# Performance work log

Hardware: AMD Instinct MI355X
Metric: run time of the kernel (lower is better)

The kernel has to match this reference:

```python
import jax, jax.numpy as jnp
import numpy as np

DIM = 256
HEADS = 8
HD = DIM // HEADS  # 32
RPE_H = 512
STRIDE = 16
B, NQ = 4, 300
HH, WW = 64, 64
N = HH * WW


def setup_inputs() -> dict:
    key = jax.random.key(0)
    ks = jax.random.split(key, 24)

    def lin(k, fan_in, fan_out):
        return (jax.random.normal(k, (fan_in, fan_out), jnp.float32)
                / np.float32(np.sqrt(fan_in)))

    # boxes in absolute pixel coords (image is WW*STRIDE = 1024 px wide)
    rp_xy = jax.random.uniform(ks[0], (B, NQ, 1, 2), jnp.float32) * (WW * STRIDE)
    rp_wh = jax.random.uniform(ks[1], (B, NQ, 1, 2), jnp.float32) * 256.0 + 16.0
    reference_points = jnp.concatenate([rp_xy, rp_wh], axis=-1)  # [B,NQ,1,4]

    inp = {
        "query": jax.random.normal(ks[2], (B, NQ, DIM), jnp.float32),
        "reference_points": reference_points,
        "k_input_flatten": jax.random.normal(ks[3], (B, N, DIM), jnp.float32),
        "v_input_flatten": jax.random.normal(ks[4], (B, N, DIM), jnp.float32),
        "input_spatial_shapes": jnp.array([[HH, WW]], dtype=jnp.int32),
        "input_padding_mask": (jax.random.uniform(ks[5], (B, N)) < 0.1).astype(jnp.int32),
        # projections (stored as [in, out]; y = x @ W + b)
        "Wq": lin(ks[6], DIM, DIM), "bq": jnp.zeros((DIM,), jnp.float32),
        "Wk": lin(ks[7], DIM, DIM), "bk": jnp.zeros((DIM,), jnp.float32),
        "Wv": lin(ks[8], DIM, DIM), "bv": jnp.zeros((DIM,), jnp.float32),
        "Wp": lin(ks[9], DIM, DIM), "bp": jnp.zeros((DIM,), jnp.float32),
        # CPB MLP 1 (x-deltas): Linear(2,512)+ReLU+Linear(512,HEADS,no bias)
        "W1x": lin(ks[10], 2, RPE_H), "b1x": jnp.zeros((RPE_H,), jnp.float32),
        "W2x": lin(ks[11], RPE_H, HEADS),
        # CPB MLP 2 (y-deltas)
        "W1y": lin(ks[12], 2, RPE_H), "b1y": jnp.zeros((RPE_H,), jnp.float32),
        "W2y": lin(ks[13], RPE_H, HEADS),
    }
    return inp


def reference(query, reference_points, k_input_flatten, v_input_flatten,
              input_spatial_shapes, input_padding_mask,
              Wq, bq, Wk, bk, Wv, bv, Wp, bp,
              W1x, b1x, W2x, W1y, b1y, W2y):
    h = int(input_spatial_shapes[0, 0])
    w = int(input_spatial_shapes[0, 1])
    scale = HD ** -0.5

    # cxcywh -> (x1,y1,x2,y2)
    c, s = reference_points[..., :2], reference_points[..., 2:]
    ref_pts = jnp.concatenate([c - s / 2, c + s / 2], axis=-1)  # [B,NQ,1,4]

    pos_x = (jnp.arange(w, dtype=jnp.float32) + 0.5) * STRIDE  # [w]
    pos_y = (jnp.arange(h, dtype=jnp.float32) + 0.5) * STRIDE  # [h]
    delta_x = ref_pts[..., 0::2] - pos_x[None, None, :, None]  # [B,NQ,w,2]
    delta_y = ref_pts[..., 1::2] - pos_y[None, None, :, None]  # [B,NQ,h,2]

    rpe_x = jax.nn.relu(delta_x @ W1x + b1x) @ W2x  # [B,NQ,w,HEADS]
    rpe_y = jax.nn.relu(delta_y @ W1y + b1y) @ W2y  # [B,NQ,h,HEADS]
    rpe = rpe_x[:, :, None, :, :] + rpe_y[:, :, :, None, :]  # [B,NQ,h,w,H]

    Bq, Nq, C = query.shape
    rpe = rpe.reshape(Bq, Nq, h * w, HEADS).transpose(0, 3, 1, 2)  # [B,H,NQ,N]

    q = (query @ Wq + bq).reshape(Bq, Nq, HEADS, HD).transpose(0, 2, 1, 3) * scale
    k = (k_input_flatten @ Wk + bk).reshape(Bq, -1, HEADS, HD).transpose(0, 2, 1, 3)
    v = (v_input_flatten @ Wv + bv).reshape(Bq, -1, HEADS, HD).transpose(0, 2, 1, 3)

    attn = jnp.einsum('bhqd,bhkd->bhqk', q, k) + rpe
    attn = attn + input_padding_mask[:, None, None, :].astype(attn.dtype) * (-100.0)
    fi = jnp.finfo(attn.dtype)
    attn = jnp.clip(attn, fi.min, fi.max)
    attn = jax.nn.softmax(attn, axis=-1)

    x = jnp.einsum('bhqk,bhkd->bhqd', attn, v)
    x = x.transpose(0, 2, 1, 3).reshape(Bq, Nq, C)
    return x @ Wp + bp
```

## Files before the change

kernel.cpp:

```cpp
#include <hip/hip_runtime.h>
#include <math.h>

#define B_   4
#define NQ_  300
#define DIM_ 256
#define H_   8
#define HD_  32
#define N_   4096

typedef _Float16 f16;
typedef f16   f16x8 __attribute__((ext_vector_type(8)));
typedef f16   f16x4 __attribute__((ext_vector_type(4)));
typedef float f32x4 __attribute__((ext_vector_type(4)));

#define L2E 1.44269504f

__global__ __launch_bounds__(256) void prep_wt(
    const float* __restrict__ Wq, const float* __restrict__ Wk,
    const float* __restrict__ Wv, const float* __restrict__ Wp,
    const int* __restrict__ mask, f16* __restrict__ WT,
    float* __restrict__ maskf, float qscale)
{
  const int z = blockIdx.z;
  if (z == 4) {
    const int flat = blockIdx.y * 4 + blockIdx.x;
    const int idx = flat * 1024 + threadIdx.x * 4;
    int4 mm = *(const int4*)(mask + idx);
    float4 o;
    o.x = -100.f * L2E * (float)mm.x;
    o.y = -100.f * L2E * (float)mm.y;
    o.z = -100.f * L2E * (float)mm.z;
    o.w = -100.f * L2E * (float)mm.w;
    *(float4*)(maskf + idx) = o;
    return;
  }
  __shared__ float t[64][65];
  const float* W = z == 0 ? Wq : z == 1 ? Wk : z == 2 ? Wv : Wp;
  const float s = z == 0 ? qscale : 1.0f;
  f16* O = WT + (size_t)z * 65536;
  const int k0 = blockIdx.y * 64, n0 = blockIdx.x * 64;
  const int r = threadIdx.x >> 2, c0 = (threadIdx.x & 3) * 16;
#pragma unroll
  for (int c = 0; c < 16; c += 4) {
    float4 v = *(const float4*)(W + (size_t)(k0 + r) * 256 + n0 + c0 + c);
    t[r][c0 + c] = v.x; t[r][c0 + c + 1] = v.y;
    t[r][c0 + c + 2] = v.z; t[r][c0 + c + 3] = v.w;
  }
  __syncthreads();
  f16* orow = O + (size_t)(n0 + r) * 256 + k0 + c0;
#pragma unroll
  for (int c = 0; c < 16; c += 4) {
    f16x4 p;
    p[0] = (f16)(t[c0 + c + 0][r] * s);
    p[1] = (f16)(t[c0 + c + 1][r] * s);
    p[2] = (f16)(t[c0 + c + 2][r] * s);
    p[3] = (f16)(t[c0 + c + 3][r] * s);
    *(f16x4*)(orow + c) = p;
  }
}

__device__ __forceinline__ void gemm_body(
    const void* __restrict__ Ain, const f16* __restrict__ WT,
    const float* __restrict__ bias, void* __restrict__ C,
    int M, int a_f16, int mode, int bm, int bn, int tid)
{
  __shared__ f16 As[128][40];
  __shared__ f16 Bs[64][40];
  __shared__ f16 Ts[64][132];
  const int lane = tid & 63;
  const int wv = tid >> 6;
  const int l15 = lane & 15, g = lane >> 4;

  f32x4 acc[2][4];
#pragma unroll
  for (int mt = 0; mt < 2; ++mt)
#pragma unroll
    for (int nt = 0; nt < 4; ++nt) acc[mt][nt] = (f32x4){0.f, 0.f, 0.f, 0.f};

  for (int k0 = 0; k0 < 256; k0 += 32) {
#pragma unroll
    for (int i = 0; i < 2; ++i) {
      const int c = tid + i * 256;
      const int row = c >> 2, k8 = (c & 3) * 8;
      const int gm = bm + row;
      f16x8 av;
      if (gm < M) {
        if (a_f16) {
          av = *(const f16x8*)((const f16*)Ain + (size_t)gm * 256 + k0 + k8);
        } else {
          const float* ap = (const float*)Ain + (size_t)gm * 256 + k0 + k8;
          float4 a0 = *(const float4*)ap;
          float4 a1 = *(const float4*)(ap + 4);
          av[0] = (f16)a0.x; av[1] = (f16)a0.y; av[2] = (f16)a0.z; av[3] = (f16)a0.w;
          av[4] = (f16)a1.x; av[5] = (f16)a1.y; av[6] = (f16)a1.z; av[7] = (f16)a1.w;
        }
      } else {
#pragma unroll
        for (int j = 0; j < 8; ++j) av[j] = (f16)0.f;
      }
      *(f16x8*)&As[row][k8] = av;
    }
    {
      const int n = tid >> 2, k8 = (tid & 3) * 8;
      *(f16x8*)&Bs[n][k8] = *(const f16x8*)(WT + (size_t)(bn + n) * 256 + k0 + k8);
    }
    __syncthreads();
    const f16x8 af0 = *(const f16x8*)&As[wv * 32 + l15][g * 8];
    const f16x8 af1 = *(const f16x8*)&As[wv * 32 + 16 + l15][g * 8];
#pragma unroll
    for (int nt = 0; nt < 4; ++nt) {
      const f16x8 bf = *(const f16x8*)&Bs[nt * 16 + l15][g * 8];
      acc[0][nt] = __builtin_amdgcn_mfma_f32_16x16x32_f16(af0, bf, acc[0][nt], 0, 0, 0);
      acc[1][nt] = __builtin_amdgcn_mfma_f32_16x16x32_f16(af1, bf, acc[1][nt], 0, 0, 0);
    }
    __syncthreads();
  }

  if (mode == 2) {
#pragma unroll
    for (int nt = 0; nt < 4; ++nt) {
      const float bv = bias[bn + nt * 16 + l15];
#pragma unroll
      for (int mt = 0; mt < 2; ++mt)
#pragma unroll
        for (int r = 0; r < 4; ++r)
          Ts[nt * 16 + l15][wv * 32 + mt * 16 + g * 4 + r] = (f16)(acc[mt][nt][r] + bv);
    }
    __syncthreads();
    const int n = tid >> 2, mc = (tid & 3) * 32;
    const int bb = bm >> 12, nk0 = bm & 4095;
    f16* dst = (f16*)C + (size_t)bb * (256 * 4096) +
               (size_t)(bn + n) * 4096 + nk0 + mc;
#pragma unroll
    for (int j = 0; j < 4; ++j)
      *(f16x8*)(dst + j * 8) = *(const f16x8*)&Ts[n][mc + j * 8];
  } else {
#pragma unroll
    for (int nt = 0; nt < 4; ++nt) {
      const int n = bn + nt * 16 + l15;
      const float bv = bias[n];
#pragma unroll
      for (int mt = 0; mt < 2; ++mt)
#pragma unroll
      for (int r = 0; r < 4; ++r) {
        const int m = bm + wv * 32 + mt * 16 + g * 4 + r;
        if (m >= M) continue;
        const float v = acc[mt][nt][r] + bv;
        if (mode == 0) ((float*)C)[(size_t)m * 256 + n] = v;
        else           ((f16*)C)[(size_t)m * 256 + n] = (f16)v;
      }
    }
  }
}

__global__ __launch_bounds__(256) void proj_qkv(
    const float* __restrict__ query, const float* __restrict__ kin,
    const float* __restrict__ vin, const f16* __restrict__ WT,
    const float* __restrict__ bq, const float* __restrict__ bk,
    const float* __restrict__ bv, f16* __restrict__ Qf,
    f16* __restrict__ Kf, f16* __restrict__ Vtf)
{
  const int z = blockIdx.z;
  const int bm = blockIdx.y * 128, bn = blockIdx.x * 64;
  if (z == 0) {
    if (bm >= B_ * NQ_) return;
    gemm_body(query, WT, bq, Qf, B_ * NQ_, 0, 1, bm, bn, threadIdx.x);
  } else if (z == 1) {
    gemm_body(kin, WT + 65536, bk, Kf, B_ * N_, 0, 1, bm, bn, threadIdx.x);
  } else {
    gemm_body(vin, WT + 2 * 65536, bv, Vtf, B_ * N_, 0, 2, bm, bn, threadIdx.x);
  }
}

__global__ __launch_bounds__(256) void gemm_out(
    const f16* __restrict__ X, const f16* __restrict__ WT,
    const float* __restrict__ bp, float* __restrict__ out)
{
  gemm_body(X, WT + 3 * 65536, bp, out, B_ * NQ_, 1, 0,
            blockIdx.y * 128, blockIdx.x * 64, threadIdx.x);
}

__global__ __launch_bounds__(256) void rpe_kernel(
    const float* __restrict__ refpts,
    const float* __restrict__ W1x, const float* __restrict__ b1x, const float* __restrict__ W2x,
    const float* __restrict__ W1y, const float* __restrict__ b1y, const float* __restrict__ W2y,
    float* __restrict__ rpxT, float* __restrict__ rpyT)
{
  __shared__ float sRed[4][64][9];
  const int tid = threadIdx.x;
  const int lane = tid & 63;
  const int wv = __builtin_amdgcn_readfirstlane(tid >> 6);
  const int bq = blockIdx.x;
  const int axis = blockIdx.y;
  const float* W1 = axis ? W1y : W1x;
  const float* b1 = axis ? b1y : b1x;
  const float* W2 = axis ? W2y : W2x;
  float* out = axis ? rpyT : rpxT;
  const int b = bq / NQ_, q = bq % NQ_;

  const float c  = refpts[bq * 4 + axis];
  const float sz = refpts[bq * 4 + 2 + axis];
  const float pos = (lane + 0.5f) * 16.0f;
  const float d0 = c - 0.5f * sz - pos;
  const float d1 = c + 0.5f * sz - pos;
  float acc[8] = {};
  const int r0 = wv * 128;
#pragma unroll 4
  for (int i = 0; i < 128; ++i) {
    const int r = r0 + i;
    const float w10 = W1[r], w11 = W1[512 + r], bb = b1[r];
    const float hv = fmaxf(fmaf(d0, w10, fmaf(d1, w11, bb)), 0.0f);
    const float* w2r = W2 + r * 8;
#pragma unroll
    for (int hh = 0; hh < 8; ++hh) acc[hh] += hv * w2r[hh];
  }
#pragma unroll
  for (int hh = 0; hh < 8; ++hh) sRed[wv][lane][hh] = acc[hh];
  __syncthreads();
  for (int idx = tid; idx < 512; idx += 256) {
    const int hh = idx >> 6, jj = idx & 63;
    out[((size_t)(b * H_ + hh) * NQ_ + q) * 64 + jj] =
        (sRed[0][jj][hh] + sRed[1][jj][hh] + sRed[2][jj][hh] + sRed[3][jj][hh]) * L2E;
  }
}

__global__ __launch_bounds__(512, 4) void attn_mfma(
    const f16* __restrict__ Qf, const f16* __restrict__ Kf,
    const f16* __restrict__ Vtf, const float* __restrict__ rpxT,
    const float* __restrict__ rpyT, const float* __restrict__ maskf,
    f16* __restrict__ X)
{
  __shared__ float srx[32][68];
  __shared__ float sry[32][68];
  __shared__ float pm[8][2][64];
  __shared__ f16x4 mO4[7][4][64];
  __shared__ float mll[7][32];

  const int tid = threadIdx.x;
  const int lane = tid & 63;
  const int kh = tid >> 6;
  const int qg = blockIdx.x % 10;
  const int h  = (blockIdx.x / 10) % H_;
  const int b  = blockIdx.x / (10 * H_);
  const int q0 = qg * 32;

  {
    const int qq = tid >> 4, j4 = tid & 15;
    int qa = q0 + qq; if (qa > NQ_ - 1) qa = NQ_ - 1;
    const size_t base = ((size_t)((b * H_ + h) * NQ_ + qa)) * 64 + j4 * 4;
    *(float4*)&srx[qq][j4 * 4] = *(const float4*)(rpxT + base);
    *(float4*)&sry[qq][j4 * 4] = *(const float4*)(rpyT + base);
  }
  __syncthreads();

  const int l15 = lane & 15, g = lane >> 4;
  const int qrow0 = q0 + l15;
  const int qrow1 = q0 + 16 + l15;
  const int qa = qrow0 > NQ_ - 1 ? NQ_ - 1 : qrow0;
  const int qb = qrow1 > NQ_ - 1 ? NQ_ - 1 : qrow1;

  const f16x8 qf0 = *(const f16x8*)(Qf + (size_t)(b * NQ_ + qa) * 256 + h * 32 + g * 8);
  const f16x8 qf1 = *(const f16x8*)(Qf + (size_t)(b * NQ_ + qb) * 256 + h * 32 + g * 8);

  const f16* kb  = Kf + (size_t)b * N_ * 256 + h * 32 + g * 8;
  const f16* v0p = Vtf + (size_t)(b * 256 + h * 32 + l15) * N_ + g * 4;
  const f16* v1p = v0p + (size_t)16 * N_;
  const float* mb = maskf + b * N_;

  float cmax0 = -1e30f, cmax1 = -1e30f;
  for (int sp = 0; sp < 8; ++sp) {
    const int kbase = kh * 512 + sp * 64;
    f16x8 kf[4]; float4 m4[4];
#pragma unroll
    for (int cc = 0; cc < 4; ++cc) {
      kf[cc] = *(const f16x8*)(kb + (size_t)(kbase + cc * 16 + l15) * 256);
      m4[cc] = *(const float4*)(mb + kbase + cc * 16 + g * 4);
    }
    const float ry0 = sry[l15][kbase >> 6];
    const float ry1 = sry[16 + l15][kbase >> 6];
#pragma unroll
    for (int cc = 0; cc < 4; ++cc) {
      f32x4 S0 = __builtin_amdgcn_mfma_f32_16x16x32_f16(
          kf[cc], qf0, (f32x4){0.f, 0.f, 0.f, 0.f}, 0, 0, 0);
      f32x4 S1 = __builtin_amdgcn_mfma_f32_16x16x32_f16(
          kf[cc], qf1, (f32x4){0.f, 0.f, 0.f, 0.f}, 0, 0, 0);
      const float4 rx0 = *(const float4*)&srx[l15][cc * 16 + g * 4];
      const float4 rx1 = *(const float4*)&srx[16 + l15][cc * 16 + g * 4];
      cmax0 = fmaxf(cmax0, fmaxf(
          fmaxf(fmaf(S0[0], L2E, rx0.x + m4[cc].x + ry0),
                fmaf(S0[1], L2E, rx0.y + m4[cc].y + ry0)),
          fmaxf(fmaf(S0[2], L2E, rx0.z + m4[cc].z + ry0),
                fmaf(S0[3], L2E, rx0.w + m4[cc].w + ry0))));
      cmax1 = fmaxf(cmax1, fmaxf(
          fmaxf(fmaf(S1[0], L2E, rx1.x + m4[cc].x + ry1),
                fmaf(S1[1], L2E, rx1.y + m4[cc].y + ry1)),
          fmaxf(fmaf(S1[2], L2E, rx1.z + m4[cc].z + ry1),
                fmaf(S1[3], L2E, rx1.w + m4[cc].w + ry1))));
    }
  }
  pm[kh][0][lane] = cmax0;
  pm[kh][1][lane] = cmax1;
  __syncthreads();
  float m0 = -1e30f, m1 = -1e30f;
#pragma unroll
  for (int w = 0; w < 8; ++w)
#pragma unroll
    for (int gg = 0; gg < 4; ++gg) {
      m0 = fmaxf(m0, pm[w][0][gg * 16 + l15]);
      m1 = fmaxf(m1, pm[w][1][gg * 16 + l15]);
    }

  f32x4 O00 = {0.f,0.f,0.f,0.f}, O01 = {0.f,0.f,0.f,0.f};
  f32x4 O10 = {0.f,0.f,0.f,0.f}, O11 = {0.f,0.f,0.f,0.f};
  float lacc0 = 0.f, lacc1 = 0.f;
  for (int sp = 0; sp < 8; ++sp) {
    const int kbase = kh * 512 + sp * 64;
    f16x8 kf[4]; f16x4 va[4], vb[4]; float4 m4[4];
#pragma unroll
    for (int cc = 0; cc < 4; ++cc) {
      kf[cc] = *(const f16x8*)(kb + (size_t)(kbase + cc * 16 + l15) * 256);
      va[cc] = *(const f16x4*)(v0p + kbase + cc * 16);
      vb[cc] = *(const f16x4*)(v1p + kbase + cc * 16);
      m4[cc] = *(const float4*)(mb + kbase + cc * 16 + g * 4);
    }
    const float ry0 = sry[l15][kbase >> 6] - m0;
    const float ry1 = sry[16 + l15][kbase >> 6] - m1;
#pragma unroll
    for (int cc = 0; cc < 4; ++cc) {
      f32x4 S0 = __builtin_amdgcn_mfma_f32_16x16x32_f16(
          kf[cc], qf0, (f32x4){0.f, 0.f, 0.f, 0.f}, 0, 0, 0);
      f32x4 S1 = __builtin_amdgcn_mfma_f32_16x16x32_f16(
          kf[cc], qf1, (f32x4){0.f, 0.f, 0.f, 0.f}, 0, 0, 0);
      const float4 rx0 = *(const float4*)&srx[l15][cc * 16 + g * 4];
      const float4 rx1 = *(const float4*)&srx[16 + l15][cc * 16 + g * 4];
      f16x4 pf0, pf1;
      {
        const float p0 = exp2f(fmaf(S0[0], L2E, rx0.x + m4[cc].x + ry0));
        const float p1 = exp2f(fmaf(S0[1], L2E, rx0.y + m4[cc].y + ry0));
        const float p2 = exp2f(fmaf(S0[2], L2E, rx0.z + m4[cc].z + ry0));
        const float p3 = exp2f(fmaf(S0[3], L2E, rx0.w + m4[cc].w + ry0));
        lacc0 += p0 + p1 + p2 + p3;
        pf0[0] = (f16)p0; pf0[1] = (f16)p1; pf0[2] = (f16)p2; pf0[3] = (f16)p3;
      }
      {
        const float p0 = exp2f(fmaf(S1[0], L2E, rx1.x + m4[cc].x + ry1));
        const float p1 = exp2f(fmaf(S1[1], L2E, rx1.y + m4[cc].y + ry1));
        const float p2 = exp2f(fmaf(S1[2], L2E, rx1.z + m4[cc].z + ry1));
        const float p3 = exp2f(fmaf(S1[3], L2E, rx1.w + m4[cc].w + ry1));
        lacc1 += p0 + p1 + p2 + p3;
        pf1[0] = (f16)p0; pf1[1] = (f16)p1; pf1[2] = (f16)p2; pf1[3] = (f16)p3;
      }
      O00 = __builtin_amdgcn_mfma_f32_16x16x16f16(va[cc], pf0, O00, 0, 0, 0);
      O01 = __builtin_amdgcn_mfma_f32_16x16x16f16(vb[cc], pf0, O01, 0, 0, 0);
      O10 = __builtin_amdgcn_mfma_f32_16x16x16f16(va[cc], pf1, O10, 0, 0, 0);
      O11 = __builtin_amdgcn_mfma_f32_16x16x16f16(vb[cc], pf1, O11, 0, 0, 0);
    }
  }
  lacc0 += __shfl_xor(lacc0, 16); lacc0 += __shfl_xor(lacc0, 32);
  lacc1 += __shfl_xor(lacc1, 16); lacc1 += __shfl_xor(lacc1, 32);

  if (kh > 0) {
    f16x4 t;
#pragma unroll
    for (int r = 0; r < 4; ++r) t[r] = (f16)O00[r];
    mO4[kh - 1][0][lane] = t;
#pragma unroll
    for (int r = 0; r < 4; ++r) t[r] = (f16)O01[r];
    mO4[kh - 1][1][lane] = t;
#pragma unroll
    for (int r = 0; r < 4; ++r) t[r] = (f16)O10[r];
    mO4[kh - 1][2][lane] = t;
#pragma unroll
    for (int r = 0; r < 4; ++r) t[r] = (f16)O11[r];
    mO4[kh - 1][3][lane] = t;
    if (lane < 16) {
      mll[kh - 1][lane]      = lacc0;
      mll[kh - 1][16 + lane] = lacc1;
    }
  }
  __syncthreads();
  if (kh == 0) {
    float lt0 = lacc0, lt1 = lacc1;
#pragma unroll
    for (int w = 0; w < 7; ++w) {
      lt0 += mll[w][l15];
      lt1 += mll[w][16 + l15];
#pragma unroll
      for (int r = 0; r < 4; ++r) {
        O00[r] += (float)mO4[w][0][lane][r];
        O01[r] += (float)mO4[w][1][lane][r];
        O10[r] += (float)mO4[w][2][lane][r];
        O11[r] += (float)mO4[w][3][lane][r];
      }
    }
    const float rl0 = 1.0f / lt0;
    const float rl1 = 1.0f / lt1;
    if (qrow0 < NQ_) {
      f16* xr = X + (size_t)(b * NQ_ + qrow0) * 256 + h * 32;
      f16x4 p0, p1;
#pragma unroll
      for (int r = 0; r < 4; ++r) {
        p0[r] = (f16)(O00[r] * rl0);
        p1[r] = (f16)(O01[r] * rl0);
      }
      *(f16x4*)(xr + g * 4) = p0;
      *(f16x4*)(xr + 16 + g * 4) = p1;
    }
    if (qrow1 < NQ_) {
      f16* xr = X + (size_t)(b * NQ_ + qrow1) * 256 + h * 32;
      f16x4 p0, p1;
#pragma unroll
      for (int r = 0; r < 4; ++r) {
        p0[r] = (f16)(O10[r] * rl1);
        p1[r] = (f16)(O11[r] * rl1);
      }
      *(f16x4*)(xr + g * 4) = p0;
      *(f16x4*)(xr + 16 + g * 4) = p1;
    }
  }
}

extern "C" void kernel_launch(void* const* d_in, const int* in_sizes, int n_in,
                              void* d_out, int out_size, void* d_ws, size_t ws_size,
                              hipStream_t stream)
{
  const float* query  = (const float*)d_in[0];
  const float* refpts = (const float*)d_in[1];
  const float* kin    = (const float*)d_in[2];
  const float* vin    = (const float*)d_in[3];
  const int*   mask   = (const int*)d_in[5];
  const float* Wq = (const float*)d_in[6];
  const float* bq = (const float*)d_in[7];
  const float* Wk = (const float*)d_in[8];
  const float* bk = (const float*)d_in[9];
  const float* Wv = (const float*)d_in[10];
  const float* bv = (const float*)d_in[11];
  const float* Wp = (const float*)d_in[12];
  const float* bp = (const float*)d_in[13];
  const float* W1x = (const float*)d_in[14];
  const float* b1x = (const float*)d_in[15];
  const float* W2x = (const float*)d_in[16];
  const float* W1y = (const float*)d_in[17];
  const float* b1y = (const float*)d_in[18];
  const float* W2y = (const float*)d_in[19];

  char* wsb = (char*)d_ws;
  f16*   Qf    = (f16*)(wsb);
  f16*   Kf    = (f16*)(wsb + 655360);
  f16*   Vtf   = (f16*)(wsb + 9043968);
  float* rpxT  = (float*)(wsb + 17432576);
  float* rpyT  = (float*)(wsb + 19890176);
  f16*   X     = (f16*)(wsb + 22347776);
  f16*   WT    = (f16*)(wsb + 23003136);
  float* maskf = (float*)(wsb + 23527424);

  const float scale = 0.17677669529663687f;

  hipLaunchKernelGGL(prep_wt, dim3(4, 4, 5), dim3(256), 0, stream,
                     Wq, Wk, Wv, Wp, mask, WT, maskf, scale);
  hipLaunchKernelGGL(rpe_kernel, dim3(B_ * NQ_, 2), dim3(256), 0, stream,
                     refpts, W1x, b1x, W2x, W1y, b1y, W2y, rpxT, rpyT);
  hipLaunchKernelGGL(proj_qkv, dim3(4, 128, 3), dim3(256), 0, stream,
                     query, kin, vin, WT, bq, bk, bv, Qf, Kf, Vtf);
  hipLaunchKernelGGL(attn_mfma, dim3(B_ * H_ * 10), dim3(512), 0, stream,
                     Qf, Kf, Vtf, rpxT, rpyT, maskf, X);
  hipLaunchKernelGGL(gemm_out, dim3(4, 10), dim3(256), 0, stream,
                     X, WT, bp, (float*)d_out);
}
```

Baseline: 251.2 us.

## Replace two-pass softmax with online softmax and split keys across two blocks

Removes the separate max-finding pass over K in the attention kernel and uses an online (running-max) softmax with rescaling, so K/QK^T are computed once instead of twice. The key range is also split between two blocks per query group, which doubles the grid to 640 blocks, and a new merge kernel combines the partial outputs using the log-sum-exp factors. Partials are written to the workspace as fp32. This adds an extra launch, per-tile rescaling work and partial-result traffic. The launch-bounds occupancy hint is dropped.

```diff
diff --git a/kernel.cpp b/kernel.cpp
--- a/kernel.cpp
+++ b/kernel.cpp
@@ -224,30 +224,33 @@
   }
 }
 
-__global__ __launch_bounds__(512, 4) void attn_mfma(
+__global__ __launch_bounds__(512) void attn_mfma(
     const f16* __restrict__ Qf, const f16* __restrict__ Kf,
     const f16* __restrict__ Vtf, const float* __restrict__ rpxT,
     const float* __restrict__ rpyT, const float* __restrict__ maskf,
-    f16* __restrict__ X)
+    float* __restrict__ pO, float* __restrict__ pml)
 {
   __shared__ float srx[32][68];
   __shared__ float sry[32][68];
-  __shared__ float pm[8][2][64];
   __shared__ f16x4 mO4[7][4][64];
+  __shared__ float mlm[7][32];
   __shared__ float mll[7][32];
 
   const int tid = threadIdx.x;
   const int lane = tid & 63;
-  const int kh = tid >> 6;
-  const int qg = blockIdx.x % 10;
-  const int h  = (blockIdx.x / 10) % H_;
-  const int b  = blockIdx.x / (10 * H_);
+  const int kw = tid >> 6;
+  const int bid = blockIdx.x;
+  const int KH = bid & 1;
+  const int rest = bid >> 1;
+  const int qg = rest % 10;
+  const int h  = (rest / 10) % H_;
+  const int b  = rest / (10 * H_);
   const int q0 = qg * 32;
 
   {
     const int qq = tid >> 4, j4 = tid & 15;
-    int qa = q0 + qq; if (qa > NQ_ - 1) qa = NQ_ - 1;
-    const size_t base = ((size_t)((b * H_ + h) * NQ_ + qa)) * 64 + j4 * 4;
+    int qa2 = q0 + qq; if (qa2 > NQ_ - 1) qa2 = NQ_ - 1;
+    const size_t base = ((size_t)((b * H_ + h) * NQ_ + qa2)) * 64 + j4 * 4;
     *(float4*)&srx[qq][j4 * 4] = *(const float4*)(rpxT + base);
     *(float4*)&sry[qq][j4 * 4] = *(const float4*)(rpyT + base);
   }
@@ -262,59 +265,17 @@
   const f16x8 qf0 = *(const f16x8*)(Qf + (size_t)(b * NQ_ + qa) * 256 + h * 32 + g * 8);
   const f16x8 qf1 = *(const f16x8*)(Qf + (size_t)(b * NQ_ + qb) * 256 + h * 32 + g * 8);
 
+  f32x4 O00 = {0.f,0.f,0.f,0.f}, O01 = {0.f,0.f,0.f,0.f};
+  f32x4 O10 = {0.f,0.f,0.f,0.f}, O11 = {0.f,0.f,0.f,0.f};
+  float lacc0 = 0.f, lacc1 = 0.f;
+  float mrun0 = -1e30f, mrun1 = -1e30f;
   const f16* kb  = Kf + (size_t)b * N_ * 256 + h * 32 + g * 8;
   const f16* v0p = Vtf + (size_t)(b * 256 + h * 32 + l15) * N_ + g * 4;
   const f16* v1p = v0p + (size_t)16 * N_;
   const float* mb = maskf + b * N_;
 
-  float cmax0 = -1e30f, cmax1 = -1e30f;
-  for (int sp = 0; sp < 8; ++sp) {
-    const int kbase = kh * 512 + sp * 64;
-    f16x8 kf[4]; float4 m4[4];
-#pragma unroll
-    for (int cc = 0; cc < 4; ++cc) {
-      kf[cc] = *(const f16x8*)(kb + (size_t)(kbase + cc * 16 + l15) * 256);
-      m4[cc] = *(const float4*)(mb + kbase + cc * 16 + g * 4);
-    }
-    const float ry0 = sry[l15][kbase >> 6];
-    const float ry1 = sry[16 + l15][kbase >> 6];
-#pragma unroll
-    for (int cc = 0; cc < 4; ++cc) {
-      f32x4 S0 = __builtin_amdgcn_mfma_f32_16x16x32_f16(
-          kf[cc], qf0, (f32x4){0.f, 0.f, 0.f, 0.f}, 0, 0, 0);
-      f32x4 S1 = __builtin_amdgcn_mfma_f32_16x16x32_f16(
-          kf[cc], qf1, (f32x4){0.f, 0.f, 0.f, 0.f}, 0, 0, 0);
-      const float4 rx0 = *(const float4*)&srx[l15][cc * 16 + g * 4];
-      const float4 rx1 = *(const float4*)&srx[16 + l15][cc * 16 + g * 4];
-      cmax0 = fmaxf(cmax0, fmaxf(
-          fmaxf(fmaf(S0[0], L2E, rx0.x + m4[cc].x + ry0),
-                fmaf(S0[1], L2E, rx0.y + m4[cc].y + ry0)),
-          fmaxf(fmaf(S0[2], L2E, rx0.z + m4[cc].z + ry0),
-                fmaf(S0[3], L2E, rx0.w + m4[cc].w + ry0))));
-      cmax1 = fmaxf(cmax1, fmaxf(
-          fmaxf(fmaf(S1[0], L2E, rx1.x + m4[cc].x + ry1),
-                fmaf(S1[1], L2E, rx1.y + m4[cc].y + ry1)),
-          fmaxf(fmaf(S1[2], L2E, rx1.z + m4[cc].z + ry1),
-                fmaf(S1[3], L2E, rx1.w + m4[cc].w + ry1))));
-    }
-  }
-  pm[kh][0][lane] = cmax0;
-  pm[kh][1][lane] = cmax1;
-  __syncthreads();
-  float m0 = -1e30f, m1 = -1e30f;
-#pragma unroll
-  for (int w = 0; w < 8; ++w)
-#pragma unroll
-    for (int gg = 0; gg < 4; ++gg) {
-      m0 = fmaxf(m0, pm[w][0][gg * 16 + l15]);
-      m1 = fmaxf(m1, pm[w][1][gg * 16 + l15]);
-    }
-
-  f32x4 O00 = {0.f,0.f,0.f,0.f}, O01 = {0.f,0.f,0.f,0.f};
-  f32x4 O10 = {0.f,0.f,0.f,0.f}, O11 = {0.f,0.f,0.f,0.f};
-  float lacc0 = 0.f, lacc1 = 0.f;
-  for (int sp = 0; sp < 8; ++sp) {
-    const int kbase = kh * 512 + sp * 64;
+  for (int sp = 0; sp < 4; ++sp) {
+    const int kbase = KH * 2048 + kw * 256 + sp * 64;
     f16x8 kf[4]; f16x4 va[4], vb[4]; float4 m4[4];
 #pragma unroll
     for (int cc = 0; cc < 4; ++cc) {
@@ -323,32 +284,53 @@
       vb[cc] = *(const f16x4*)(v1p + kbase + cc * 16);
       m4[cc] = *(const float4*)(mb + kbase + cc * 16 + g * 4);
     }
-    const float ry0 = sry[l15][kbase >> 6] - m0;
-    const float ry1 = sry[16 + l15][kbase >> 6] - m1;
+    f32x4 s0[4], s1[4];
+    float lm0 = -1e30f, lm1 = -1e30f;
+    const float ry0 = sry[l15][kbase >> 6];
+    const float ry1 = sry[16 + l15][kbase >> 6];
 #pragma unroll
     for (int cc = 0; cc < 4; ++cc) {
       f32x4 S0 = __builtin_amdgcn_mfma_f32_16x16x32_f16(
-          kf[cc], qf0, (f32x4){0.f, 0.f, 0.f, 0.f}, 0, 0, 0);
+          kf[cc], qf0, (f32x4){0.f,0.f,0.f,0.f}, 0, 0, 0);
       f32x4 S1 = __builtin_amdgcn_mfma_f32_16x16x32_f16(
-          kf[cc], qf1, (f32x4){0.f, 0.f, 0.f, 0.f}, 0, 0, 0);
+          kf[cc], qf1, (f32x4){0.f,0.f,0.f,0.f}, 0, 0, 0);
       const float4 rx0 = *(const float4*)&srx[l15][cc * 16 + g * 4];
       const float4 rx1 = *(const float4*)&srx[16 + l15][cc * 16 + g * 4];
+      s0[cc][0] = fmaf(S0[0], L2E, rx0.x + m4[cc].x + ry0);
+      s0[cc][1] = fmaf(S0[1], L2E, rx0.y + m4[cc].y + ry0);
+      s0[cc][2] = fmaf(S0[2], L2E, rx0.z + m4[cc].z + ry0);
+      s0[cc][3] = fmaf(S0[3], L2E, rx0.w + m4[cc].w + ry0);
+      s1[cc][0] = fmaf(S1[0], L2E, rx1.x + m4[cc].x + ry1);
+      s1[cc][1] = fmaf(S1[1], L2E, rx1.y + m4[cc].y + ry1);
+      s1[cc][2] = fmaf(S1[2], L2E, rx1.z + m4[cc].z + ry1);
+      s1[cc][3] = fmaf(S1[3], L2E, rx1.w + m4[cc].w + ry1);
+      lm0 = fmaxf(lm0, fmaxf(fmaxf(s0[cc][0], s0[cc][1]), fmaxf(s0[cc][2], s0[cc][3])));
+      lm1 = fmaxf(lm1, fmaxf(fmaxf(s1[cc][0], s1[cc][1]), fmaxf(s1[cc][2], s1[cc][3])));
+    }
+    lm0 = fmaxf(lm0, __shfl_xor(lm0, 16));
+    lm0 = fmaxf(lm0, __shfl_xor(lm0, 32));
+    lm1 = fmaxf(lm1, __shfl_xor(lm1, 16));
+    lm1 = fmaxf(lm1, __shfl_xor(lm1, 32));
+    const float mn0 = fmaxf(mrun0, lm0);
+    const float mn1 = fmaxf(mrun1, lm1);
+    const float f0 = exp2f(mrun0 - mn0);
+    const float f1 = exp2f(mrun1 - mn1);
+    mrun0 = mn0; mrun1 = mn1;
+    lacc0 *= f0; lacc1 *= f1;
+#pragma unroll
+    for (int r = 0; r < 4; ++r) {
+      O00[r] *= f0; O01[r] *= f0;
+      O10[r] *= f1; O11[r] *= f1;
+    }
+#pragma unroll
+    for (int cc = 0; cc < 4; ++cc) {
       f16x4 pf0, pf1;
-      {
-        const float p0 = exp2f(fmaf(S0[0], L2E, rx0.x + m4[cc].x + ry0));
-        const float p1 = exp2f(fmaf(S0[1], L2E, rx0.y + m4[cc].y + ry0));
-        const float p2 = exp2f(fmaf(S0[2], L2E, rx0.z + m4[cc].z + ry0));
-        const float p3 = exp2f(fmaf(S0[3], L2E, rx0.w + m4[cc].w + ry0));
-        lacc0 += p0 + p1 + p2 + p3;
-        pf0[0] = (f16)p0; pf0[1] = (f16)p1; pf0[2] = (f16)p2; pf0[3] = (f16)p3;
-      }
-      {
-        const float p0 = exp2f(fmaf(S1[0], L2E, rx1.x + m4[cc].x + ry1));
-        const float p1 = exp2f(fmaf(S1[1], L2E, rx1.y + m4[cc].y + ry1));
-        const float p2 = exp2f(fmaf(S1[2], L2E, rx1.z + m4[cc].z + ry1));
-        const float p3 = exp2f(fmaf(S1[3], L2E, rx1.w + m4[cc].w + ry1));
-        lacc1 += p0 + p1 + p2 + p3;
-        pf1[0] = (f16)p0; pf1[1] = (f16)p1; pf1[2] = (f16)p2; pf1[3] = (f16)p3;
+#pragma unroll
+      for (int r = 0; r < 4; ++r) {
+        const float p0 = exp2f(s0[cc][r] - mrun0);
+        const float p1 = exp2f(s1[cc][r] - mrun1);
+        lacc0 += p0; lacc1 += p1;
+        pf0[r] = (f16)p0; pf1[r] = (f16)p1;
       }
       O00 = __builtin_amdgcn_mfma_f32_16x16x16f16(va[cc], pf0, O00, 0, 0, 0);
       O01 = __builtin_amdgcn_mfma_f32_16x16x16f16(vb[cc], pf0, O01, 0, 0, 0);
@@ -356,67 +338,107 @@
       O11 = __builtin_amdgcn_mfma_f32_16x16x16f16(vb[cc], pf1, O11, 0, 0, 0);
     }
   }
+
   lacc0 += __shfl_xor(lacc0, 16); lacc0 += __shfl_xor(lacc0, 32);
   lacc1 += __shfl_xor(lacc1, 16); lacc1 += __shfl_xor(lacc1, 32);
 
-  if (kh > 0) {
+  if (kw > 0) {
     f16x4 t;
 #pragma unroll
     for (int r = 0; r < 4; ++r) t[r] = (f16)O00[r];
-    mO4[kh - 1][0][lane] = t;
+    mO4[kw - 1][0][lane] = t;
 #pragma unroll
     for (int r = 0; r < 4; ++r) t[r] = (f16)O01[r];
-    mO4[kh - 1][1][lane] = t;
+    mO4[kw - 1][1][lane] = t;
 #pragma unroll
     for (int r = 0; r < 4; ++r) t[r] = (f16)O10[r];
-    mO4[kh - 1][2][lane] = t;
+    mO4[kw - 1][2][lane] = t;
 #pragma unroll
     for (int r = 0; r < 4; ++r) t[r] = (f16)O11[r];
-    mO4[kh - 1][3][lane] = t;
+    mO4[kw - 1][3][lane] = t;
     if (lane < 16) {
-      mll[kh - 1][lane]      = lacc0;
-      mll[kh - 1][16 + lane] = lacc1;
+      mlm[kw - 1][lane]      = mrun0;
+      mlm[kw - 1][16 + lane] = mrun1;
+      mll[kw - 1][lane]      = lacc0;
+      mll[kw - 1][16 + lane] = lacc1;
     }
   }
   __syncthreads();
-  if (kh == 0) {
-    float lt0 = lacc0, lt1 = lacc1;
+  if (kw == 0) {
+    float ms0 = mrun0, ms1 = mrun1;
 #pragma unroll
     for (int w = 0; w < 7; ++w) {
-      lt0 += mll[w][l15];
-      lt1 += mll[w][16 + l15];
+      ms0 = fmaxf(ms0, mlm[w][l15]);
+      ms1 = fmaxf(ms1, mlm[w][16 + l15]);
+    }
+    const float fs0 = exp2f(mrun0 - ms0);
+    const float fs1 = exp2f(mrun1 - ms1);
+    float lt0 = lacc0 * fs0, lt1 = lacc1 * fs1;
+#pragma unroll
+    for (int r = 0; r < 4; ++r) {
+      O00[r] *= fs0; O01[r] *= fs0;
+      O10[r] *= fs1; O11[r] *= fs1;
+    }
+#pragma unroll
+    for (int w = 0; w < 7; ++w) {
+      const float fw0 = exp2f(mlm[w][l15] - ms0);
+      const float fw1 = exp2f(mlm[w][16 + l15] - ms1);
+      lt0 += mll[w][l15] * fw0;
+      lt1 += mll[w][16 + l15] * fw1;
 #pragma unroll
       for (int r = 0; r < 4; ++r) {
-        O00[r] += (float)mO4[w][0][lane][r];
-        O01[r] += (float)mO4[w][1][lane][r];
-        O10[r] += (float)mO4[w][2][lane][r];
-        O11[r] += (float)mO4[w][3][lane][r];
+        O00[r] += (float)mO4[w][0][lane][r] * fw0;
+        O01[r] += (float)mO4[w][1][lane][r] * fw0;
+        O10[r] += (float)mO4[w][2][lane][r] * fw1;
+        O11[r] += (float)mO4[w][3][lane][r] * fw1;
       }
     }
-    const float rl0 = 1.0f / lt0;
-    const float rl1 = 1.0f / lt1;
-    if (qrow0 < NQ_) {
-      f16* xr = X + (size_t)(b * NQ_ + qrow0) * 256 + h * 32;
-      f16x4 p0, p1;
-#pragma unroll
-      for (int r = 0; r < 4; ++r) {
-        p0[r] = (f16)(O00[r] * rl0);
-        p1[r] = (f16)(O01[r] * rl0);
-      }
-      *(f16x4*)(xr + g * 4) = p0;
-      *(f16x4*)(xr + 16 + g * 4) = p1;
-    }
-    if (qrow1 < NQ_) {
-      f16* xr = X + (size_t)(b * NQ_ + qrow1) * 256 + h * 32;
-      f16x4 p0, p1;
-#pragma unroll
-      for (int r = 0; r < 4; ++r) {
-        p0[r] = (f16)(O10[r] * rl1);
-        p1[r] = (f16)(O11[r] * rl1);
-      }
-      *(f16x4*)(xr + g * 4) = p0;
-      *(f16x4*)(xr + 16 + g * 4) = p1;
-    }
+    float4* pO4 = (float4*)pO;
+    const size_t pb2 = ((size_t)rest * 2 + KH) * 4 * 64;
+    pO4[pb2 + 0 * 64 + lane] = make_float4(O00[0], O00[1], O00[2], O00[3]);
+    pO4[pb2 + 1 * 64 + lane] = make_float4(O01[0], O01[1], O01[2], O01[3]);
+    pO4[pb2 + 2 * 64 + lane] = make_float4(O10[0], O10[1], O10[2], O10[3]);
+    pO4[pb2 + 3 * 64 + lane] = make_float4(O11[0], O11[1], O11[2], O11[3]);
+    if (lane < 16) {
+      float* pp = pml + ((size_t)rest * 2 + KH) * 64;
+      pp[l15]      = ms0;
+      pp[16 + l15] = lt0;
+      pp[32 + l15] = ms1;
+      pp[48 + l15] = lt1;
+    }
+  }
+}
+
+__global__ __launch_bounds__(256) void attn_merge(
+    const float* __restrict__ pO, const float* __restrict__ pml,
+    f16* __restrict__ X)
+{
+  const int pb = blockIdx.x;
+  const int qg = pb % 10;
+  const int h  = (pb / 10) % H_;
+  const int b  = pb / (10 * H_);
+  const int t = threadIdx.x;
+  const int qt = t >> 7, oh = (t >> 6) & 1, lane = t & 63;
+  const int l15 = lane & 15, g = lane >> 4;
+
+  const float4* pO4 = (const float4*)pO;
+  const float4 a = pO4[(((size_t)pb * 2 + 0) * 4 + qt * 2 + oh) * 64 + lane];
+  const float4 c = pO4[(((size_t)pb * 2 + 1) * 4 + qt * 2 + oh) * 64 + lane];
+  const float* pp0 = pml + ((size_t)pb * 2 + 0) * 64 + qt * 32;
+  const float* pp1 = pml + ((size_t)pb * 2 + 1) * 64 + qt * 32;
+  const float m0 = pp0[l15], l0 = pp0[16 + l15];
+  const float m1 = pp1[l15], l1 = pp1[16 + l15];
+  const float ms = fmaxf(m0, m1);
+  const float f0 = exp2f(m0 - ms), f1 = exp2f(m1 - ms);
+  const float rl = 1.0f / (l0 * f0 + l1 * f1);
+  const int qrow = qg * 32 + qt * 16 + l15;
+  if (qrow < NQ_) {
+    f16x4 o;
+    o[0] = (f16)((a.x * f0 + c.x * f1) * rl);
+    o[1] = (f16)((a.y * f0 + c.y * f1) * rl);
+    o[2] = (f16)((a.z * f0 + c.z * f1) * rl);
+    o[3] = (f16)((a.w * f0 + c.w * f1) * rl);
+    *(f16x4*)(X + (size_t)(b * NQ_ + qrow) * 256 + h * 32 + oh * 16 + g * 4) = o;
   }
 }
 
@@ -453,6 +475,8 @@
   f16*   X     = (f16*)(wsb + 22347776);
   f16*   WT    = (f16*)(wsb + 23003136);
   float* maskf = (float*)(wsb + 23527424);
+  float* pO    = (float*)(wsb + 23592960);
+  float* pml   = (float*)(wsb + 26214400);
 
   const float scale = 0.17677669529663687f;
 
@@ -462,8 +486,10 @@
                      refpts, W1x, b1x, W2x, W1y, b1y, W2y, rpxT, rpyT);
   hipLaunchKernelGGL(proj_qkv, dim3(4, 128, 3), dim3(256), 0, stream,
                      query, kin, vin, WT, bq, bk, bv, Qf, Kf, Vtf);
-  hipLaunchKernelGGL(attn_mfma, dim3(B_ * H_ * 10), dim3(512), 0, stream,
-                     Qf, Kf, Vtf, rpxT, rpyT, maskf, X);
+  hipLaunchKernelGGL(attn_mfma, dim3(B_ * H_ * 10 * 2), dim3(512), 0, stream,
+                     Qf, Kf, Vtf, rpxT, rpyT, maskf, pO, pml);
+  hipLaunchKernelGGL(attn_merge, dim3(B_ * H_ * 10), dim3(256), 0, stream,
+                     pO, pml, X);
   hipLaunchKernelGGL(gemm_out, dim3(4, 10), dim3(256), 0, stream,
                      X, WT, bp, (float*)d_out);
 }
```

Result: faster. 226.3 us (-9.9%).
